# Performance work log

Measured on AMD Instinct MI355X. Metric: run time of the kernel, lower is better.

The kernel has to match this reference:

```python
import jax, jax.numpy as jnp
import numpy as np

NEG_SLOPE = 0.2  # PyG GATConv default negative_slope


def gat_conv(x, src, dst, W, a_src, a_dst, b):
    """PyG GATConv with concat=False (mean over heads). src/dst include self-loops."""
    N = x.shape[0]
    H, C = a_src.shape
    h = (x @ W).reshape(N, H, C)                      # [N,H,C]
    alpha_src = (h * a_src).sum(-1)                   # [N,H]
    alpha_dst = (h * a_dst).sum(-1)                   # [N,H]
    e = jax.nn.leaky_relu(alpha_src[src] + alpha_dst[dst], NEG_SLOPE)  # [E,H]
    # segment softmax over incoming edges of each dst node
    emax = jax.ops.segment_max(e, dst, num_segments=N)                 # [N,H]
    ex = jnp.exp(e - emax[dst])                                        # [E,H]
    denom = jax.ops.segment_sum(ex, dst, num_segments=N)               # [N,H]
    alpha = ex / denom[dst]                                            # [E,H]
    msg = h[src] * alpha[:, :, None]                                   # [E,H,C]
    out = jax.ops.segment_sum(msg, dst, num_segments=N)                # [N,H,C]
    return out.mean(axis=1) + b                                        # concat=False -> mean heads


def setup_inputs() -> dict:
    key = jax.random.key(0)
    ks = jax.random.split(key, 16)
    N, F_IN, H, C, E = 50000, 3, 4, 64, 800000
    inp = {
        "x": jax.random.normal(ks[0], (N, F_IN), dtype=jnp.float32),
        "edge_index": jax.random.randint(ks[1], (2, E), 0, N, dtype=jnp.int32),
        "W1": jax.random.normal(ks[2], (F_IN, H * C), dtype=jnp.float32) * 0.1,
        "a1_src": jax.random.normal(ks[3], (H, C), dtype=jnp.float32) * 0.1,
        "a1_dst": jax.random.normal(ks[4], (H, C), dtype=jnp.float32) * 0.1,
        "b1": jnp.zeros((C,), dtype=jnp.float32),
        "W2": jax.random.normal(ks[5], (C, H * C), dtype=jnp.float32) * 0.1,
        "a2_src": jax.random.normal(ks[6], (H, C), dtype=jnp.float32) * 0.1,
        "a2_dst": jax.random.normal(ks[7], (H, C), dtype=jnp.float32) * 0.1,
        "b2": jnp.zeros((C,), dtype=jnp.float32),
        "W3": jax.random.normal(ks[8], (C, H * C), dtype=jnp.float32) * 0.1,
        "a3_src": jax.random.normal(ks[9], (H, C), dtype=jnp.float32) * 0.1,
        "a3_dst": jax.random.normal(ks[10], (H, C), dtype=jnp.float32) * 0.1,
        "b3": jnp.zeros((C,), dtype=jnp.float32),
        "lin_w": jax.random.normal(ks[11], (C, 1), dtype=jnp.float32) * 0.1,
        "lin_b": jnp.zeros((1,), dtype=jnp.float32),
    }
    return inp


def reference(x, edge_index, W1, a1_src, a1_dst, b1, W2, a2_src, a2_dst, b2,
              W3, a3_src, a3_dst, b3, lin_w, lin_b):
    N = x.shape[0]
    loops = jnp.arange(N, dtype=edge_index.dtype)  # PyG add_self_loops=True default
    src = jnp.concatenate([edge_index[0], loops])
    dst = jnp.concatenate([edge_index[1], loops])

    h1 = jax.nn.elu(gat_conv(x, src, dst, W1, a1_src, a1_dst, b1))
    h2 = jax.nn.elu(gat_conv(h1, src, dst, W2, a2_src, a2_dst, b2)) + h1
    h3 = jax.nn.elu(gat_conv(h2, src, dst, W3, a3_src, a3_dst, b3)) + h2
    return h3 @ lin_w + lin_b
```

## Files before the change

### kernel.cpp

```cpp
#include <hip/hip_runtime.h>
#include <math.h>

#define HEADS 4
#define CH 64
#define HC 256

typedef __attribute__((ext_vector_type(8))) short bf16x8;
typedef __attribute__((ext_vector_type(4))) float f32x4;

__device__ __forceinline__ float lrelu(float v) { return v > 0.f ? v : 0.2f * v; }

__device__ __forceinline__ unsigned int f2bf(float f) {
    unsigned int u = __float_as_uint(f);
    u += 0x7fffu + ((u >> 16) & 1u);
    return u >> 16;
}
__device__ __forceinline__ float bf2f(unsigned short u) {
    return __uint_as_float(((unsigned int)u) << 16);
}

__device__ __forceinline__ float4 wave_sum4(float4 v) {
#pragma unroll
    for (int m = 32; m; m >>= 1) {
        v.x += __shfl_xor(v.x, m);
        v.y += __shfl_xor(v.y, m);
        v.z += __shfl_xor(v.z, m);
        v.w += __shfl_xor(v.w, m);
    }
    return v;
}

__global__ void count_kernel(const int* __restrict__ dst, int E, int vec_ok,
                             float scale8, int* __restrict__ deg) {
    int r = blockIdx.x & 7;
    int i = (blockIdx.x >> 3) * blockDim.x + threadIdx.x;
    int e0 = i * 4;
    if (e0 >= E) return;
    int d[4];
    int cnt;
    if (vec_ok && e0 + 3 < E) {
        int4 v = *(const int4*)(dst + e0);
        d[0] = v.x; d[1] = v.y; d[2] = v.z; d[3] = v.w; cnt = 4;
    } else {
        cnt = min(4, E - e0);
        for (int k = 0; k < cnt; ++k) d[k] = dst[e0 + k];
    }
    for (int k = 0; k < cnt; ++k) {
        int rr = min(7, (int)((float)d[k] * scale8));
        if (rr == r) atomicAdd(&deg[d[k]], 1);
    }
}

__global__ void scan_blocks(const int* __restrict__ deg,
                            int* __restrict__ off,
                            int* __restrict__ bsum,
                            const float* __restrict__ x,
                            float4* __restrict__ xq, int N) {
    __shared__ int sh[256];
    int t = threadIdx.x;
    int g = blockIdx.x * 256 + t;
    int v = (g < N) ? deg[g] + 1 : 0;
    if (g < N) xq[g] = make_float4(x[3 * g], x[3 * g + 1], x[3 * g + 2], 0.f);
    sh[t] = v;
    __syncthreads();
    for (int d = 1; d < 256; d <<= 1) {
        int xv = (t >= d) ? sh[t - d] : 0;
        __syncthreads();
        sh[t] += xv;
        __syncthreads();
    }
    if (g < N) off[g] = sh[t] - v;
    if (t == 255) bsum[blockIdx.x] = sh[255];
}

__global__ void scan_bsums(int* __restrict__ bsum, int G,
                           int* __restrict__ total_out) {
    __shared__ int sh[256];
    int t = threadIdx.x;
    int chunk = (G + 255) / 256;
    int lo = t * chunk, hi = min(lo + chunk, G);
    int s = 0;
    for (int i = lo; i < hi; ++i) s += bsum[i];
    sh[t] = s;
    __syncthreads();
    for (int d = 1; d < 256; d <<= 1) {
        int xv = (t >= d) ? sh[t - d] : 0;
        __syncthreads();
        sh[t] += xv;
        __syncthreads();
    }
    int run = (t > 0) ? sh[t - 1] : 0;
    for (int i = lo; i < hi; ++i) { int v = bsum[i]; bsum[i] = run; run += v; }
    if (t == 255) *total_out = sh[255];
}

__global__ void scan_add(int* __restrict__ off, const int* __restrict__ bsum,
                         const int* __restrict__ deg,
                         int* __restrict__ csr_src, int N) {
    int g = blockIdx.x * 256 + threadIdx.x;
    if (g < N) {
        int o = off[g] + bsum[blockIdx.x];
        off[g] = o;
        csr_src[o + deg[g]] = g;
    }
}

__global__ void scatter_kernel(const int* __restrict__ src,
                               const int* __restrict__ dst, int E, int vec_ok,
                               float scale8,
                               const int* __restrict__ off,
                               int* __restrict__ cursor,
                               int* __restrict__ csr_src) {
    int r = blockIdx.x & 7;
    int i = (blockIdx.x >> 3) * blockDim.x + threadIdx.x;
    int e0 = i * 4;
    if (e0 >= E) return;
    int s[4], d[4];
    int cnt;
    if (vec_ok && e0 + 3 < E) {
        int4 sv = *(const int4*)(src + e0);
        int4 dv = *(const int4*)(dst + e0);
        s[0] = sv.x; s[1] = sv.y; s[2] = sv.z; s[3] = sv.w;
        d[0] = dv.x; d[1] = dv.y; d[2] = dv.z; d[3] = dv.w; cnt = 4;
    } else {
        cnt = min(4, E - e0);
        for (int k = 0; k < cnt; ++k) { s[k] = src[e0 + k]; d[k] = dst[e0 + k]; }
    }
    for (int k = 0; k < cnt; ++k) {
        int rr = min(7, (int)((float)d[k] * scale8));
        if (rr != r) continue;
        int p = atomicAdd(&cursor[d[k]], 1);
        csr_src[off[d[k]] + p] = s[k];
    }
}

__device__ __forceinline__ void prep_blk(int b, int t, const float* W,
                                         const float* a_s, const float* a_d,
                                         unsigned short* Wb, float* ws,
                                         float* wd) {
    if (b < 64) {
        Wb[b * 256 + t] = (unsigned short)f2bf(W[(t >> 2) * HC + (t & 3) * CH + b]);
    } else {
        int idx = (b - 64) * 256 + t;
        int which = idx >= 256;
        int i = which ? idx - 256 : idx;
        int k = i >> 2, h = i & 3;
        const float* av = (which ? a_d : a_s) + h * CH;
        const float* Wr = W + (size_t)k * HC + h * CH;
        float s = 0.f;
        for (int c = 0; c < CH; ++c) s += Wr[c] * av[c];
        (which ? wd : ws)[i] = s;
    }
}

__global__ void prep_all(const float* __restrict__ W1,
                         const float* __restrict__ a1s,
                         const float* __restrict__ a1d,
                         float* __restrict__ ws1, float* __restrict__ wd1,
                         const float* __restrict__ W2,
                         const float* __restrict__ a2s,
                         const float* __restrict__ a2d,
                         unsigned short* __restrict__ Wb2,
                         float* __restrict__ ws2, float* __restrict__ wd2,
                         const float* __restrict__ W3,
                         const float* __restrict__ a3s,
                         const float* __restrict__ a3d,
                         unsigned short* __restrict__ Wb3,
                         float* __restrict__ ws3, float* __restrict__ wd3) {
    int b = blockIdx.x, t = threadIdx.x;
    if (b < 66) {
        prep_blk(b, t, W2, a2s, a2d, Wb2, ws2, wd2);
    } else if (b < 132) {
        prep_blk(b - 66, t, W3, a3s, a3d, Wb3, ws3, wd3);
    } else {
        for (int idx = t; idx < 24; idx += blockDim.x) {
            int which = idx >= 12;
            int i = which ? idx - 12 : idx;
            int k = i >> 2, h = i & 3;
            const float* av = (which ? a1d : a1s) + h * CH;
            const float* Wr = W1 + (size_t)k * HC + h * CH;
            float s = 0.f;
            for (int c = 0; c < CH; ++c) s += Wr[c] * av[c];
            (which ? wd1 : ws1)[i] = s;
        }
    }
}

__global__ void fused1_kernel(const int* __restrict__ off,
                              const int* __restrict__ csr_src,
                              const float4* __restrict__ xq,
                              const float* __restrict__ ws,
                              const float* __restrict__ wd,
                              float4* __restrict__ zl, int N) {
    int t = blockIdx.x * blockDim.x + threadIdx.x;
    int n = t >> 2, j = t & 3;
    if (n >= N) return;
    float4 xn = xq[n];
    float ad0 = xn.x * wd[0] + xn.y * wd[4] + xn.z * wd[8];
    float ad1 = xn.x * wd[1] + xn.y * wd[5] + xn.z * wd[9];
    float ad2 = xn.x * wd[2] + xn.y * wd[6] + xn.z * wd[10];
    float ad3 = xn.x * wd[3] + xn.y * wd[7] + xn.z * wd[11];

    int o0 = off[n], o1 = off[n + 1];
    float z[12];
#pragma unroll
    for (int q = 0; q < 12; ++q) z[q] = 0.f;
    float l0 = 0.f, l1 = 0.f, l2 = 0.f, l3 = 0.f;

    for (int i = o0 + j; i < o1; i += 4) {
        int s = csr_src[i];
        float4 xv = xq[s];
        float e0 = __expf(lrelu(xv.x * ws[0] + xv.y * ws[4] + xv.z * ws[8]  + ad0));
        float e1 = __expf(lrelu(xv.x * ws[1] + xv.y * ws[5] + xv.z * ws[9]  + ad1));
        float e2 = __expf(lrelu(xv.x * ws[2] + xv.y * ws[6] + xv.z * ws[10] + ad2));
        float e3 = __expf(lrelu(xv.x * ws[3] + xv.y * ws[7] + xv.z * ws[11] + ad3));
        l0 += e0; l1 += e1; l2 += e2; l3 += e3;
        z[0] += e0 * xv.x; z[1]  += e0 * xv.y; z[2]  += e0 * xv.z;
        z[3] += e1 * xv.x; z[4]  += e1 * xv.y; z[5]  += e1 * xv.z;
        z[6] += e2 * xv.x; z[7]  += e2 * xv.y; z[8]  += e2 * xv.z;
        z[9] += e3 * xv.x; z[10] += e3 * xv.y; z[11] += e3 * xv.z;
    }
#pragma unroll
    for (int m = 1; m < 4; m <<= 1) {
#pragma unroll
        for (int q = 0; q < 12; ++q) z[q] += __shfl_xor(z[q], m);
        l0 += __shfl_xor(l0, m);
        l1 += __shfl_xor(l1, m);
        l2 += __shfl_xor(l2, m);
        l3 += __shfl_xor(l3, m);
    }
    if (j == 0) {
        zl[(size_t)n * 4 + 0] = make_float4(z[0], z[1], z[2], z[3]);
        zl[(size_t)n * 4 + 1] = make_float4(z[4], z[5], z[6], z[7]);
        zl[(size_t)n * 4 + 2] = make_float4(z[8], z[9], z[10], z[11]);
        zl[(size_t)n * 4 + 3] = make_float4(l0, l1, l2, l3);
    }
}

__global__ void epi1_kernel(const float4* __restrict__ zl,
                            const float* __restrict__ W1,
                            const float* __restrict__ b1,
                            const float4* __restrict__ ws2_4,
                            const float4* __restrict__ wd2_4,
                            float4* __restrict__ asrc4,
                            float4* __restrict__ adst4,
                            float* __restrict__ out,
                            unsigned short* __restrict__ out_pack, int N) {
    int node = (blockIdx.x * blockDim.x + threadIdx.x) >> 6;
    int c = threadIdx.x & 63;
    if (node >= N) return;
    float4 z0 = zl[(size_t)node * 4 + 0];
    float4 z1 = zl[(size_t)node * 4 + 1];
    float4 z2 = zl[(size_t)node * 4 + 2];
    float4 l4 = zl[(size_t)node * 4 + 3];
    float i0 = 0.25f / l4.x, i1 = 0.25f / l4.y;
    float i2 = 0.25f / l4.z, i3 = 0.25f / l4.w;
    float acc =
        (z0.x * W1[0 * HC +   0 + c] + z0.y * W1[1 * HC +   0 + c] + z0.z * W1[2 * HC +   0 + c]) * i0 +
        (z0.w * W1[0 * HC +  64 + c] + z1.x * W1[1 * HC +  64 + c] + z1.y * W1[2 * HC +  64 + c]) * i1 +
        (z1.z * W1[0 * HC + 128 + c] + z1.w * W1[1 * HC + 128 + c] + z2.x * W1[2 * HC + 128 + c]) * i2 +
        (z2.y * W1[0 * HC + 192 + c] + z2.z * W1[1 * HC + 192 + c] + z2.w * W1[2 * HC + 192 + c]) * i3;
    float v = acc + b1[c];
    v = v > 0.f ? v : expm1f(v);
    out[(size_t)node * CH + c] = v;
    out_pack[(size_t)node * CH + c] = (unsigned short)f2bf(v);
    float4 wsv = ws2_4[c], wdv = wd2_4[c];
    float4 sacc = make_float4(v * wsv.x, v * wsv.y, v * wsv.z, v * wsv.w);
    float4 dacc = make_float4(v * wdv.x, v * wdv.y, v * wdv.z, v * wdv.w);
    sacc = wave_sum4(sacc);
    dacc = wave_sum4(dacc);
    if (c == 0) { asrc4[node] = sacc; adst4[node] = dacc; }
}

__global__ __launch_bounds__(512) void layer_fused(
                            const int* __restrict__ off,
                            const int* __restrict__ csr_src,
                            const unsigned short* __restrict__ xp,
                            const float4* __restrict__ asrc4,
                            const float4* __restrict__ adst4,
                            const unsigned short* __restrict__ Wb,
                            const float* __restrict__ bias,
                            const float* __restrict__ residual,
                            const float4* __restrict__ wsn4,
                            const float4* __restrict__ wdn4,
                            float4* __restrict__ oasrc4,
                            float4* __restrict__ oadst4,
                            const float* __restrict__ lin_w,
                            const float* __restrict__ lin_b,
                            float* __restrict__ out_f32,
                            unsigned short* __restrict__ out_pack,
                            float* __restrict__ out_final, int N) {
    __shared__ unsigned short zs[32][256];
    __shared__ float4 exs[8][64];
    __shared__ unsigned int sss[8][64];

    int w = threadIdx.x >> 6;
    int lane = threadIdx.x & 63;
    const char* xpb = (const char*)xp + lane * 2;
    char* zbase = (char*)zs;

    for (int ii = 0; ii < 4; ++ii) {
        int rloc = w * 4 + ii;
        int node = blockIdx.x * 32 + rloc;
        if (node < N) {
            int o0 = off[node], o1 = off[node + 1];
            int deg = o1 - o0;
            float4 ad = adst4[node];
            float l0 = 0.f, l1 = 0.f, l2 = 0.f, l3 = 0.f;
            float z0 = 0.f, z1 = 0.f, z2 = 0.f, z3 = 0.f;
            for (int base = 0; base < deg; base += 64) {
                int i = base + lane;
                int s = 0;
                float4 ev = make_float4(-INFINITY, -INFINITY, -INFINITY, -INFINITY);
                if (i < deg) {
                    s = csr_src[o0 + i];
                    float4 as = asrc4[s];
                    ev.x = lrelu(as.x + ad.x);
                    ev.y = lrelu(as.y + ad.y);
                    ev.z = lrelu(as.z + ad.z);
                    ev.w = lrelu(as.w + ad.w);
                }
                float4 ex;
                ex.x = __expf(ev.x);
                ex.y = __expf(ev.y);
                ex.z = __expf(ev.z);
                ex.w = __expf(ev.w);
                float4 ls = wave_sum4(ex);
                l0 += ls.x; l1 += ls.y; l2 += ls.z; l3 += ls.w;
                exs[w][lane] = ex;
                sss[w][lane] = (unsigned)s * 128u;
                int cnt = min(64, deg - base);
#pragma unroll 4
                for (int e = 0; e < cnt; ++e) {
                    unsigned soff = sss[w][e];
                    float4 exe = exs[w][e];
                    float xk = bf2f(*(const unsigned short*)(xpb + soff));
                    z0 += exe.x * xk; z1 += exe.y * xk;
                    z2 += exe.z * xk; z3 += exe.w * xk;
                }
            }
            float s0 = 0.25f / l0, s1 = 0.25f / l1;
            float s2 = 0.25f / l2, s3 = 0.25f / l3;
            uint2 zo;
            zo.x = f2bf(z0 * s0) | (f2bf(z1 * s1) << 16);
            zo.y = f2bf(z2 * s2) | (f2bf(z3 * s3) << 16);
            *(uint2*)(zbase + (size_t)rloc * 512 +
                      (((unsigned)lane * 8u) ^ ((unsigned)(rloc & 7) << 4))) = zo;
        }
    }

    __syncthreads();
    if (w >= 2) return;

    int quad = lane >> 4, col = lane & 15;
    int nbase = blockIdx.x * 32 + w * 16;

    f32x4 zero4 = {0.f, 0.f, 0.f, 0.f};
    f32x4 acc[4];
#pragma unroll
    for (int t = 0; t < 4; ++t) acc[t] = zero4;

    const char* abase = (const char*)zs + (size_t)(w * 16 + col) * 512;
    unsigned aswz = (unsigned)((col & 7) << 4);
#pragma unroll
    for (int q = 0; q < 8; ++q) {
        bf16x8 af = *(const bf16x8*)(abase + (((unsigned)(quad * 16 + q * 64)) ^ aswz));
#pragma unroll
        for (int t = 0; t < 4; ++t) {
            const unsigned short* bp = Wb + (size_t)(t * 16 + col) * HC + q * 32 + quad * 8;
            bf16x8 bfrag = *(const bf16x8*)bp;
            acc[t] = __builtin_amdgcn_mfma_f32_16x16x32_bf16(af, bfrag, acc[t], 0, 0, 0);
        }
    }

    if (!out_final) {
        float vv[4][4];
#pragma unroll
        for (int t = 0; t < 4; ++t) {
            int c = t * 16 + col;
            float bc = bias[c];
#pragma unroll
            for (int r = 0; r < 4; ++r) {
                int n = nbase + quad * 4 + r;
                float v = acc[t][r] + bc;
                v = v > 0.f ? v : expm1f(v);
                v += residual[(size_t)n * CH + c];
                vv[t][r] = v;
                if (n < N) {
                    out_f32[(size_t)n * CH + c] = v;
                    out_pack[(size_t)n * CH + c] = (unsigned short)f2bf(v);
                }
            }
        }
        float4 wsv[4], wdv[4];
#pragma unroll
        for (int t = 0; t < 4; ++t) { wsv[t] = wsn4[t * 16 + col]; wdv[t] = wdn4[t * 16 + col]; }
#pragma unroll
        for (int r = 0; r < 4; ++r) {
            int n = nbase + quad * 4 + r;
            float4 sa = make_float4(0.f, 0.f, 0.f, 0.f);
            float4 da = make_float4(0.f, 0.f, 0.f, 0.f);
#pragma unroll
            for (int t = 0; t < 4; ++t) {
                float v = vv[t][r];
                sa.x += v * wsv[t].x; sa.y += v * wsv[t].y;
                sa.z += v * wsv[t].z; sa.w += v * wsv[t].w;
                da.x += v * wdv[t].x; da.y += v * wdv[t].y;
                da.z += v * wdv[t].z; da.w += v * wdv[t].w;
            }
#pragma unroll
            for (int m = 8; m; m >>= 1) {
                sa.x += __shfl_xor(sa.x, m); sa.y += __shfl_xor(sa.y, m);
                sa.z += __shfl_xor(sa.z, m); sa.w += __shfl_xor(sa.w, m);
                da.x += __shfl_xor(da.x, m); da.y += __shfl_xor(da.y, m);
                da.z += __shfl_xor(da.z, m); da.w += __shfl_xor(da.w, m);
            }
            if (col == 0 && n < N) { oasrc4[n] = sa; oadst4[n] = da; }
        }
    } else {
        float lw[4], bb[4];
#pragma unroll
        for (int t = 0; t < 4; ++t) { lw[t] = lin_w[t * 16 + col]; bb[t] = bias[t * 16 + col]; }
#pragma unroll
        for (int r = 0; r < 4; ++r) {
            int n = nbase + quad * 4 + r;
            float ts = 0.f;
#pragma unroll
            for (int t = 0; t < 4; ++t) {
                float v = acc[t][r] + bb[t];
                v = v > 0.f ? v : expm1f(v);
                v += residual[(size_t)n * CH + (t * 16 + col)];
                ts += v * lw[t];
            }
            ts += __shfl_xor(ts, 1);
            ts += __shfl_xor(ts, 2);
            ts += __shfl_xor(ts, 4);
            ts += __shfl_xor(ts, 8);
            if (col == 0 && n < N) out_final[n] = ts + lin_b[0];
        }
    }
}

extern "C" void kernel_launch(void* const* d_in, const int* in_sizes, int n_in,
                              void* d_out, int out_size, void* d_ws, size_t ws_size,
                              hipStream_t stream) {
    const float* x      = (const float*)d_in[0];
    const int*   ei     = (const int*)  d_in[1];
    const float* W1     = (const float*)d_in[2];
    const float* a1s    = (const float*)d_in[3];
    const float* a1d    = (const float*)d_in[4];
    const float* b1     = (const float*)d_in[5];
    const float* W2     = (const float*)d_in[6];
    const float* a2s    = (const float*)d_in[7];
    const float* a2d    = (const float*)d_in[8];
    const float* b2     = (const float*)d_in[9];
    const float* W3     = (const float*)d_in[10];
    const float* a3s    = (const float*)d_in[11];
    const float* a3d    = (const float*)d_in[12];
    const float* b3     = (const float*)d_in[13];
    const float* lin_w  = (const float*)d_in[14];
    const float* lin_b  = (const float*)d_in[15];

    const int N = in_sizes[0] / 3;
    const int E = in_sizes[1] / 2;
    const int Et = E + N;
    const int* src = ei;
    const int* dst = ei + E;
    const float scale8 = 8.0f / (float)N;
    const int vec_ok = ((((size_t)src | (size_t)dst) & 15) == 0) ? 1 : 0;

    float* xq_f   = (float*)d_ws;
    unsigned short* xpA = (unsigned short*)(xq_f + (size_t)N * 4);
    unsigned short* xpB = xpA + (size_t)N * CH;
    unsigned short* Wb2 = xpB + (size_t)N * CH;
    unsigned short* Wb3 = Wb2 + 16384;
    float* bufA   = (float*)(Wb3 + 16384);
    float* bufB   = bufA + (size_t)N * CH;
    float* zl     = bufB + (size_t)N * CH;
    float* asrcA  = zl   + (size_t)N * 16;
    float* adstA  = asrcA + (size_t)N * 4;
    float* asrcB  = adstA + (size_t)N * 4;
    float* adstB  = asrcB + (size_t)N * 4;
    float* ws1    = adstB + (size_t)N * 4;
    float* wd1    = ws1 + 16;
    float* ws2    = wd1 + 16;
    float* wd2    = ws2 + 256;
    float* ws3    = wd2 + 256;
    float* wd3    = ws3 + 256;
    int* deg      = (int*)(wd3 + 256);
    int* cursor   = deg + N;
    int* off      = cursor + N;
    int* bsum     = off + N + 4;
    int* csr_src  = bsum + 256;

    const int B = 256;
    const int G = (N + 255) / 256;
    const int EB4 = (E + 3) / 4;
    const int CB = (EB4 + B - 1) / B;

    hipMemsetAsync(deg, 0, (size_t)2 * N * sizeof(int), stream);
    count_kernel<<<CB * 8, B, 0, stream>>>(dst, E, vec_ok, scale8, deg);
    scan_blocks<<<G, B, 0, stream>>>(deg, off, bsum, x, (float4*)xq_f, N);
    scan_bsums<<<1, B, 0, stream>>>(bsum, G, off + N);
    scan_add<<<G, B, 0, stream>>>(off, bsum, deg, csr_src, N);
    scatter_kernel<<<CB * 8, B, 0, stream>>>(src, dst, E, vec_ok, scale8,
                                             off, cursor, csr_src);

    prep_all<<<133, B, 0, stream>>>(W1, a1s, a1d, ws1, wd1,
                                    W2, a2s, a2d, Wb2, ws2, wd2,
                                    W3, a3s, a3d, Wb3, ws3, wd3);

    int nwave_blocks = (N * 64 + B - 1) / B;
    int nfused_blocks = (N + 31) / 32;

    fused1_kernel<<<(N * 4 + B - 1) / B, B, 0, stream>>>(
        off, csr_src, (const float4*)xq_f, ws1, wd1, (float4*)zl, N);
    epi1_kernel<<<nwave_blocks, B, 0, stream>>>(
        (const float4*)zl, W1, b1, (const float4*)ws2, (const float4*)wd2,
        (float4*)asrcA, (float4*)adstA, bufA, xpA, N);

    layer_fused<<<nfused_blocks, 512, 0, stream>>>(
        off, csr_src, xpA, (const float4*)asrcA, (const float4*)adstA,
        Wb2, b2, bufA, (const float4*)ws3, (const float4*)wd3,
        (float4*)asrcB, (float4*)adstB,
        nullptr, nullptr, bufB, xpB, nullptr, N);

    layer_fused<<<nfused_blocks, 512, 0, stream>>>(
        off, csr_src, xpB, (const float4*)asrcB, (const float4*)adstB,
        Wb3, b3, bufB, nullptr, nullptr,
        nullptr, nullptr,
        lin_w, lin_b, nullptr, nullptr, (float*)d_out, N);
}
```

Before: 351.8 us.

## Split fused aggregate+GEMM layer into separate aggregation and MFMA GEMM kernels

The fused per-layer kernel, in which only two of eight waves ran the MFMA GEMM after a block barrier, is replaced by two kernels. The first is a one-wave-per-node aggregation kernel that writes bf16 aggregated features to a global buffer. The second is a standalone MFMA GEMM with the same epilogue, using all four waves per block. This removes the idle-wave tail and the barrier and gives better occupancy in each phase. In exchange, the intermediate z buffer (N x 256 bf16) makes an extra round trip through global memory, and there is one more launch per layer. The attention buffers are also reused in place between layers.

```diff
diff --git a/kernel.cpp b/kernel.cpp
--- a/kernel.cpp
+++ b/kernel.cpp
@@ -182,6 +182,168 @@
             float s = 0.f;
             for (int c = 0; c < CH; ++c) s += Wr[c] * av[c];
             (which ? wd1 : ws1)[i] = s;
+        }
+    }
+}
+
+__global__ void agg_kernel(const int* __restrict__ off,
+                           const int* __restrict__ csr_src,
+                           const unsigned short* __restrict__ xp,
+                           const float4* __restrict__ asrc4,
+                           const float4* __restrict__ adst4,
+                           uint2* __restrict__ zb2, int N) {
+    __shared__ float4 exs[4][64];
+    __shared__ unsigned int sss[4][64];
+    int node = (blockIdx.x * blockDim.x + threadIdx.x) >> 6;
+    int w = (threadIdx.x >> 6) & 3;
+    int lane = threadIdx.x & 63;
+    if (node >= N) return;
+    int o0 = off[node], o1 = off[node + 1];
+    int deg = o1 - o0;
+    float4 ad = adst4[node];
+
+    float l0 = 0.f, l1 = 0.f, l2 = 0.f, l3 = 0.f;
+    float z0 = 0.f, z1 = 0.f, z2 = 0.f, z3 = 0.f;
+    const char* xpb = (const char*)xp + lane * 2;
+
+    for (int base = 0; base < deg; base += 64) {
+        int i = base + lane;
+        int s = 0;
+        float4 ev = make_float4(-INFINITY, -INFINITY, -INFINITY, -INFINITY);
+        if (i < deg) {
+            s = csr_src[o0 + i];
+            float4 as = asrc4[s];
+            ev.x = lrelu(as.x + ad.x);
+            ev.y = lrelu(as.y + ad.y);
+            ev.z = lrelu(as.z + ad.z);
+            ev.w = lrelu(as.w + ad.w);
+        }
+        float4 ex;
+        ex.x = __expf(ev.x);
+        ex.y = __expf(ev.y);
+        ex.z = __expf(ev.z);
+        ex.w = __expf(ev.w);
+        float4 ls = wave_sum4(ex);
+        l0 += ls.x; l1 += ls.y; l2 += ls.z; l3 += ls.w;
+        exs[w][lane] = ex;
+        sss[w][lane] = (unsigned)s * 128u;
+
+        int cnt = min(64, deg - base);
+#pragma unroll 4
+        for (int e = 0; e < cnt; ++e) {
+            unsigned soff = sss[w][e];
+            float4 exe = exs[w][e];
+            float xk = bf2f(*(const unsigned short*)(xpb + soff));
+            z0 += exe.x * xk; z1 += exe.y * xk;
+            z2 += exe.z * xk; z3 += exe.w * xk;
+        }
+    }
+    float s0 = 0.25f / l0, s1 = 0.25f / l1, s2 = 0.25f / l2, s3 = 0.25f / l3;
+    uint2 zo;
+    zo.x = f2bf(z0 * s0) | (f2bf(z1 * s1) << 16);
+    zo.y = f2bf(z2 * s2) | (f2bf(z3 * s3) << 16);
+    zb2[(size_t)node * CH + lane] = zo;
+}
+
+__global__ void gemm_mfma(const unsigned short* __restrict__ zb,
+                          const unsigned short* __restrict__ Wb,
+                          const float* __restrict__ bias,
+                          const float* __restrict__ residual,
+                          const float4* __restrict__ wsn4,
+                          const float4* __restrict__ wdn4,
+                          float4* __restrict__ asrc4,
+                          float4* __restrict__ adst4,
+                          const float* __restrict__ lin_w,
+                          const float* __restrict__ lin_b,
+                          float* __restrict__ out_f32,
+                          unsigned short* __restrict__ out_pack,
+                          float* __restrict__ out_final, int N) {
+    int w = threadIdx.x >> 6;
+    int lane = threadIdx.x & 63;
+    int quad = lane >> 4, col = lane & 15;
+    int nbase = blockIdx.x * 64 + w * 16;
+
+    f32x4 zero4 = {0.f, 0.f, 0.f, 0.f};
+    f32x4 acc[4];
+#pragma unroll
+    for (int t = 0; t < 4; ++t) acc[t] = zero4;
+
+    const unsigned short* arow = zb + (size_t)(nbase + col) * HC + quad * 8;
+#pragma unroll
+    for (int q = 0; q < 8; ++q) {
+        bf16x8 af = *(const bf16x8*)(arow + q * 32);
+#pragma unroll
+        for (int t = 0; t < 4; ++t) {
+            const unsigned short* bp = Wb + (size_t)(t * 16 + col) * HC + q * 32 + quad * 8;
+            bf16x8 bfrag = *(const bf16x8*)bp;
+            acc[t] = __builtin_amdgcn_mfma_f32_16x16x32_bf16(af, bfrag, acc[t], 0, 0, 0);
+        }
+    }
+
+    if (!out_final) {
+        float vv[4][4];
+#pragma unroll
+        for (int t = 0; t < 4; ++t) {
+            int c = t * 16 + col;
+            float bc = bias[c];
+#pragma unroll
+            for (int r = 0; r < 4; ++r) {
+                int n = nbase + quad * 4 + r;
+                float v = acc[t][r] + bc;
+                v = v > 0.f ? v : expm1f(v);
+                v += residual[(size_t)n * CH + c];
+                vv[t][r] = v;
+                if (n < N) {
+                    out_f32[(size_t)n * CH + c] = v;
+                    out_pack[(size_t)n * CH + c] = (unsigned short)f2bf(v);
+                }
+            }
+        }
+        float4 wsv[4], wdv[4];
+#pragma unroll
+        for (int t = 0; t < 4; ++t) { wsv[t] = wsn4[t * 16 + col]; wdv[t] = wdn4[t * 16 + col]; }
+#pragma unroll
+        for (int r = 0; r < 4; ++r) {
+            int n = nbase + quad * 4 + r;
+            float4 sa = make_float4(0.f, 0.f, 0.f, 0.f);
+            float4 da = make_float4(0.f, 0.f, 0.f, 0.f);
+#pragma unroll
+            for (int t = 0; t < 4; ++t) {
+                float v = vv[t][r];
+                sa.x += v * wsv[t].x; sa.y += v * wsv[t].y;
+                sa.z += v * wsv[t].z; sa.w += v * wsv[t].w;
+                da.x += v * wdv[t].x; da.y += v * wdv[t].y;
+                da.z += v * wdv[t].z; da.w += v * wdv[t].w;
+            }
+#pragma unroll
+            for (int m = 8; m; m >>= 1) {
+                sa.x += __shfl_xor(sa.x, m); sa.y += __shfl_xor(sa.y, m);
+                sa.z += __shfl_xor(sa.z, m); sa.w += __shfl_xor(sa.w, m);
+                da.x += __shfl_xor(da.x, m); da.y += __shfl_xor(da.y, m);
+                da.z += __shfl_xor(da.z, m); da.w += __shfl_xor(da.w, m);
+            }
+            if (col == 0 && n < N) { asrc4[n] = sa; adst4[n] = da; }
+        }
+    } else {
+        float lw[4], bb[4];
+#pragma unroll
+        for (int t = 0; t < 4; ++t) { lw[t] = lin_w[t * 16 + col]; bb[t] = bias[t * 16 + col]; }
+#pragma unroll
+        for (int r = 0; r < 4; ++r) {
+            int n = nbase + quad * 4 + r;
+            float ts = 0.f;
+#pragma unroll
+            for (int t = 0; t < 4; ++t) {
+                float v = acc[t][r] + bb[t];
+                v = v > 0.f ? v : expm1f(v);
+                v += residual[(size_t)n * CH + (t * 16 + col)];
+                ts += v * lw[t];
+            }
+            ts += __shfl_xor(ts, 1);
+            ts += __shfl_xor(ts, 2);
+            ts += __shfl_xor(ts, 4);
+            ts += __shfl_xor(ts, 8);
+            if (col == 0 && n < N) out_final[n] = ts + lin_b[0];
         }
     }
 }
@@ -272,175 +434,6 @@
     if (c == 0) { asrc4[node] = sacc; adst4[node] = dacc; }
 }
 
-__global__ __launch_bounds__(512) void layer_fused(
-                            const int* __restrict__ off,
-                            const int* __restrict__ csr_src,
-                            const unsigned short* __restrict__ xp,
-                            const float4* __restrict__ asrc4,
-                            const float4* __restrict__ adst4,
-                            const unsigned short* __restrict__ Wb,
-                            const float* __restrict__ bias,
-                            const float* __restrict__ residual,
-                            const float4* __restrict__ wsn4,
-                            const float4* __restrict__ wdn4,
-                            float4* __restrict__ oasrc4,
-                            float4* __restrict__ oadst4,
-                            const float* __restrict__ lin_w,
-                            const float* __restrict__ lin_b,
-                            float* __restrict__ out_f32,
-                            unsigned short* __restrict__ out_pack,
-                            float* __restrict__ out_final, int N) {
-    __shared__ unsigned short zs[32][256];
-    __shared__ float4 exs[8][64];
-    __shared__ unsigned int sss[8][64];
-
-    int w = threadIdx.x >> 6;
-    int lane = threadIdx.x & 63;
-    const char* xpb = (const char*)xp + lane * 2;
-    char* zbase = (char*)zs;
-
-    for (int ii = 0; ii < 4; ++ii) {
-        int rloc = w * 4 + ii;
-        int node = blockIdx.x * 32 + rloc;
-        if (node < N) {
-            int o0 = off[node], o1 = off[node + 1];
-            int deg = o1 - o0;
-            float4 ad = adst4[node];
-            float l0 = 0.f, l1 = 0.f, l2 = 0.f, l3 = 0.f;
-            float z0 = 0.f, z1 = 0.f, z2 = 0.f, z3 = 0.f;
-            for (int base = 0; base < deg; base += 64) {
-                int i = base + lane;
-                int s = 0;
-                float4 ev = make_float4(-INFINITY, -INFINITY, -INFINITY, -INFINITY);
-                if (i < deg) {
-                    s = csr_src[o0 + i];
-                    float4 as = asrc4[s];
-                    ev.x = lrelu(as.x + ad.x);
-                    ev.y = lrelu(as.y + ad.y);
-                    ev.z = lrelu(as.z + ad.z);
-                    ev.w = lrelu(as.w + ad.w);
-                }
-                float4 ex;
-                ex.x = __expf(ev.x);
-                ex.y = __expf(ev.y);
-                ex.z = __expf(ev.z);
-                ex.w = __expf(ev.w);
-                float4 ls = wave_sum4(ex);
-                l0 += ls.x; l1 += ls.y; l2 += ls.z; l3 += ls.w;
-                exs[w][lane] = ex;
-                sss[w][lane] = (unsigned)s * 128u;
-                int cnt = min(64, deg - base);
-#pragma unroll 4
-                for (int e = 0; e < cnt; ++e) {
-                    unsigned soff = sss[w][e];
-                    float4 exe = exs[w][e];
-                    float xk = bf2f(*(const unsigned short*)(xpb + soff));
-                    z0 += exe.x * xk; z1 += exe.y * xk;
-                    z2 += exe.z * xk; z3 += exe.w * xk;
-                }
-            }
-            float s0 = 0.25f / l0, s1 = 0.25f / l1;
-            float s2 = 0.25f / l2, s3 = 0.25f / l3;
-            uint2 zo;
-            zo.x = f2bf(z0 * s0) | (f2bf(z1 * s1) << 16);
-            zo.y = f2bf(z2 * s2) | (f2bf(z3 * s3) << 16);
-            *(uint2*)(zbase + (size_t)rloc * 512 +
-                      (((unsigned)lane * 8u) ^ ((unsigned)(rloc & 7) << 4))) = zo;
-        }
-    }
-
-    __syncthreads();
-    if (w >= 2) return;
-
-    int quad = lane >> 4, col = lane & 15;
-    int nbase = blockIdx.x * 32 + w * 16;
-
-    f32x4 zero4 = {0.f, 0.f, 0.f, 0.f};
-    f32x4 acc[4];
-#pragma unroll
-    for (int t = 0; t < 4; ++t) acc[t] = zero4;
-
-    const char* abase = (const char*)zs + (size_t)(w * 16 + col) * 512;
-    unsigned aswz = (unsigned)((col & 7) << 4);
-#pragma unroll
-    for (int q = 0; q < 8; ++q) {
-        bf16x8 af = *(const bf16x8*)(abase + (((unsigned)(quad * 16 + q * 64)) ^ aswz));
-#pragma unroll
-        for (int t = 0; t < 4; ++t) {
-            const unsigned short* bp = Wb + (size_t)(t * 16 + col) * HC + q * 32 + quad * 8;
-            bf16x8 bfrag = *(const bf16x8*)bp;
-            acc[t] = __builtin_amdgcn_mfma_f32_16x16x32_bf16(af, bfrag, acc[t], 0, 0, 0);
-        }
-    }
-
-    if (!out_final) {
-        float vv[4][4];
-#pragma unroll
-        for (int t = 0; t < 4; ++t) {
-            int c = t * 16 + col;
-            float bc = bias[c];
-#pragma unroll
-            for (int r = 0; r < 4; ++r) {
-                int n = nbase + quad * 4 + r;
-                float v = acc[t][r] + bc;
-                v = v > 0.f ? v : expm1f(v);
-                v += residual[(size_t)n * CH + c];
-                vv[t][r] = v;
-                if (n < N) {
-                    out_f32[(size_t)n * CH + c] = v;
-                    out_pack[(size_t)n * CH + c] = (unsigned short)f2bf(v);
-                }
-            }
-        }
-        float4 wsv[4], wdv[4];
-#pragma unroll
-        for (int t = 0; t < 4; ++t) { wsv[t] = wsn4[t * 16 + col]; wdv[t] = wdn4[t * 16 + col]; }
-#pragma unroll
-        for (int r = 0; r < 4; ++r) {
-            int n = nbase + quad * 4 + r;
-            float4 sa = make_float4(0.f, 0.f, 0.f, 0.f);
-            float4 da = make_float4(0.f, 0.f, 0.f, 0.f);
-#pragma unroll
-            for (int t = 0; t < 4; ++t) {
-                float v = vv[t][r];
-                sa.x += v * wsv[t].x; sa.y += v * wsv[t].y;
-                sa.z += v * wsv[t].z; sa.w += v * wsv[t].w;
-                da.x += v * wdv[t].x; da.y += v * wdv[t].y;
-                da.z += v * wdv[t].z; da.w += v * wdv[t].w;
-            }
-#pragma unroll
-            for (int m = 8; m; m >>= 1) {
-                sa.x += __shfl_xor(sa.x, m); sa.y += __shfl_xor(sa.y, m);
-                sa.z += __shfl_xor(sa.z, m); sa.w += __shfl_xor(sa.w, m);
-                da.x += __shfl_xor(da.x, m); da.y += __shfl_xor(da.y, m);
-                da.z += __shfl_xor(da.z, m); da.w += __shfl_xor(da.w, m);
-            }
-            if (col == 0 && n < N) { oasrc4[n] = sa; oadst4[n] = da; }
-        }
-    } else {
-        float lw[4], bb[4];
-#pragma unroll
-        for (int t = 0; t < 4; ++t) { lw[t] = lin_w[t * 16 + col]; bb[t] = bias[t * 16 + col]; }
-#pragma unroll
-        for (int r = 0; r < 4; ++r) {
-            int n = nbase + quad * 4 + r;
-            float ts = 0.f;
-#pragma unroll
-            for (int t = 0; t < 4; ++t) {
-                float v = acc[t][r] + bb[t];
-                v = v > 0.f ? v : expm1f(v);
-                v += residual[(size_t)n * CH + (t * 16 + col)];
-                ts += v * lw[t];
-            }
-            ts += __shfl_xor(ts, 1);
-            ts += __shfl_xor(ts, 2);
-            ts += __shfl_xor(ts, 4);
-            ts += __shfl_xor(ts, 8);
-            if (col == 0 && n < N) out_final[n] = ts + lin_b[0];
-        }
-    }
-}
-
 extern "C" void kernel_launch(void* const* d_in, const int* in_sizes, int n_in,
                               void* d_out, int out_size, void* d_ws, size_t ws_size,
                               hipStream_t stream) {
@@ -470,18 +463,17 @@
     const int vec_ok = ((((size_t)src | (size_t)dst) & 15) == 0) ? 1 : 0;
 
     float* xq_f   = (float*)d_ws;
-    unsigned short* xpA = (unsigned short*)(xq_f + (size_t)N * 4);
+    unsigned short* zb  = (unsigned short*)(xq_f + (size_t)N * 4);
+    unsigned short* xpA = zb  + (size_t)N * HC;
     unsigned short* xpB = xpA + (size_t)N * CH;
     unsigned short* Wb2 = xpB + (size_t)N * CH;
     unsigned short* Wb3 = Wb2 + 16384;
     float* bufA   = (float*)(Wb3 + 16384);
     float* bufB   = bufA + (size_t)N * CH;
     float* zl     = bufB + (size_t)N * CH;
-    float* asrcA  = zl   + (size_t)N * 16;
-    float* adstA  = asrcA + (size_t)N * 4;
-    float* asrcB  = adstA + (size_t)N * 4;
-    float* adstB  = asrcB + (size_t)N * 4;
-    float* ws1    = adstB + (size_t)N * 4;
+    float* asrc   = zl   + (size_t)N * 16;
+    float* adst   = asrc + (size_t)N * 4;
+    float* ws1    = adst + (size_t)N * 4;
     float* wd1    = ws1 + 16;
     float* ws2    = wd1 + 16;
     float* wd2    = ws2 + 256;
@@ -511,23 +503,26 @@
                                     W3, a3s, a3d, Wb3, ws3, wd3);
 
     int nwave_blocks = (N * 64 + B - 1) / B;
-    int nfused_blocks = (N + 31) / 32;
+    int ngemm_blocks = (N + 63) / 64;
 
     fused1_kernel<<<(N * 4 + B - 1) / B, B, 0, stream>>>(
         off, csr_src, (const float4*)xq_f, ws1, wd1, (float4*)zl, N);
     epi1_kernel<<<nwave_blocks, B, 0, stream>>>(
         (const float4*)zl, W1, b1, (const float4*)ws2, (const float4*)wd2,
-        (float4*)asrcA, (float4*)adstA, bufA, xpA, N);
-
-    layer_fused<<<nfused_blocks, 512, 0, stream>>>(
-        off, csr_src, xpA, (const float4*)asrcA, (const float4*)adstA,
-        Wb2, b2, bufA, (const float4*)ws3, (const float4*)wd3,
-        (float4*)asrcB, (float4*)adstB,
+        (float4*)asrc, (float4*)adst, bufA, xpA, N);
+
+    agg_kernel<<<nwave_blocks, B, 0, stream>>>(
+        off, csr_src, xpA, (const float4*)asrc, (const float4*)adst,
+        (uint2*)zb, N);
+    gemm_mfma<<<ngemm_blocks, B, 0, stream>>>(
+        zb, Wb2, b2, bufA, (const float4*)ws3, (const float4*)wd3,
+        (float4*)asrc, (float4*)adst,
         nullptr, nullptr, bufB, xpB, nullptr, N);
 
-    layer_fused<<<nfused_blocks, 512, 0, stream>>>(
-        off, csr_src, xpB, (const float4*)asrcB, (const float4*)adstB,
-        Wb3, b3, bufB, nullptr, nullptr,
-        nullptr, nullptr,
+    agg_kernel<<<nwave_blocks, B, 0, stream>>>(
+        off, csr_src, xpB, (const float4*)asrc, (const float4*)adst,
+        (uint2*)zb, N);
+    gemm_mfma<<<ngemm_blocks, B, 0, stream>>>(
+        zb, Wb3, b3, bufB, nullptr, nullptr, nullptr, nullptr,
         lin_w, lin_b, nullptr, nullptr, (float*)d_out, N);
 }
```

New measurement: 344.5 us. 2.1% less time.
